# Optimization experiments

Hardware: AMD Instinct MI355X
Metric: run time of the kernel (lower is better)

The kernel has to match this reference:

```python
import jax, jax.numpy as jnp
import numpy as np

B, S, D, H = 2, 2048, 1024, 16
EPS = 1e-7  # keras backend epsilon

def setup_inputs() -> dict:
    key = jax.random.key(0)
    ks = jax.random.split(key, 5)
    x = jax.random.normal(ks[0], (B, S, D), dtype=jnp.float32)
    # mem_mask convention: attend where mem_mask == 0 (causal here)
    i = jnp.arange(S)
    causal = (i[None, :] > i[:, None]).astype(jnp.float32)  # 1 = masked
    mem_mask = jnp.broadcast_to(causal[None, None], (B, 1, S, S))
    Wqkv = jax.random.normal(ks[1], (D, 3 * D), dtype=jnp.float32) * (D ** -0.5)
    W_out = jax.random.normal(ks[2], (D, D), dtype=jnp.float32) * (D ** -0.5)
    b_out = jnp.zeros((D,), dtype=jnp.float32)
    scale = jnp.ones((D,), dtype=jnp.float32)
    gate = jax.random.normal(ks[3], (D,), dtype=jnp.float32) * 0.02
    return {"x": x, "mem_mask": mem_mask, "Wqkv": Wqkv, "W_out": W_out,
            "b_out": b_out, "scale": scale, "gate": gate}

def reference(x, mem_mask, Wqkv, W_out, b_out, scale, gate):
    b, s, d = x.shape
    dh = d // H
    h = jnp.einsum('bsd,de->bse', x, Wqkv)
    q, k, v = jnp.split(h, 3, axis=-1)
    def split_heads(t):
        return t.reshape(b, s, H, dh).transpose(0, 2, 1, 3)  # [B,H,S,dh]
    q, k, v = split_heads(q), split_heads(k), split_heads(v)
    q = q * (dh ** -0.5)
    logits = jnp.einsum('bhqd,bhkd->bhqk', q, k)
    logits = logits * (mem_mask == 0.0).astype(logits.dtype)
    weights = jax.nn.relu(logits)
    o = jnp.einsum('bhqk,bhkd->bhqd', weights, v)
    o = o.transpose(0, 2, 1, 3).reshape(b, s, d)  # combine heads
    # Gated RMSNorm
    ms = jnp.mean(o * o, axis=-1, keepdims=True)
    o = scale * o * jax.lax.rsqrt(ms + EPS) * jax.nn.sigmoid(gate * o)
    return jnp.einsum('bsd,de->bse', o, W_out) + b_out
```

## Files before the change

### kernel.cpp

```cpp
#include <hip/hip_runtime.h>
#include <hip/hip_bf16.h>

typedef unsigned short u16;
typedef __attribute__((ext_vector_type(8))) short bf16x8;
typedef __attribute__((ext_vector_type(4))) short short4v;
typedef __attribute__((ext_vector_type(4))) float floatx4;
typedef __attribute__((ext_vector_type(2))) unsigned uint2v;

__device__ __forceinline__ float bf2f(u16 u) {
    unsigned v = ((unsigned)u) << 16;
    return __builtin_bit_cast(float, v);
}
__device__ __forceinline__ u16 f2bf(float f) {
    unsigned u = __builtin_bit_cast(unsigned, f);
    u += 0x7fffu + ((u >> 16) & 1u);
    return (u16)(u >> 16);
}

#define GLDS16(g, l)                                                             \
    __builtin_amdgcn_global_load_lds(                                            \
        (const __attribute__((address_space(1))) void*)(g),                      \
        (__attribute__((address_space(3))) void*)(l), 16, 0, 0)

__global__ __launch_bounds__(256) void prep(const float* __restrict__ x, u16* __restrict__ xb,
                                            const float* __restrict__ Wqkv, u16* __restrict__ WqkvT,
                                            const float* __restrict__ Wout, u16* __restrict__ WoutT) {
    __shared__ u16 t[32][33];
    int blk = blockIdx.x;
    if (blk < 4096) {
        const int i = blk * 256 + threadIdx.x;
        const floatx4 v = ((const floatx4*)x)[i];
        short4v o;
#pragma unroll
        for (int j = 0; j < 4; ++j) o[j] = (short)f2bf(v[j]);
        ((short4v*)xb)[i] = o;
        return;
    }
    const float* in; u16* out; int R, C, bx, by;
    if (blk < 4096 + 3072) { blk -= 4096; in = Wqkv; out = WqkvT; R = 1024; C = 3072; bx = blk % 96; by = blk / 96; }
    else                   { blk -= 7168; in = Wout; out = WoutT; R = 1024; C = 1024; bx = blk & 31; by = blk >> 5; }
    const int c0 = bx * 32, r0 = by * 32;
    const int xx = threadIdx.x & 31, yy = threadIdx.x >> 5;
#pragma unroll
    for (int i = 0; i < 32; i += 8) t[yy + i][xx] = f2bf(in[(size_t)(r0 + yy + i) * C + c0 + xx]);
    __syncthreads();
#pragma unroll
    for (int i = 0; i < 32; i += 8) out[(size_t)(c0 + yy + i) * R + r0 + xx] = t[xx][yy + i];
}

template <int TM, bool BIAS, typename OUT, bool VT>
__global__ __launch_bounds__(256) void gemm_bt(const u16* __restrict__ A, const u16* __restrict__ Bt,
                                               OUT* __restrict__ C, const float* __restrict__ bias,
                                               u16* __restrict__ vtp, int M, int N, int K) {
    constexpr int MI = TM / 32;
    __shared__ u16 sA[TM * 32];
    __shared__ u16 sB[128 * 32];
    const int tid = threadIdx.x;
    const int lane = tid & 63, wave = tid >> 6;
    const int l15 = lane & 15, quad = lane >> 4;
    const int row0 = blockIdx.y * TM, col0 = blockIdx.x * 128;
    const int wm = (wave & 1) * (TM / 2), wn = (wave >> 1) * 64;
    const int c_ = (tid & 3) << 3;
    floatx4 acc[MI][4] = {};
    for (int k0 = 0; k0 < K; k0 += 32) {
#pragma unroll
        for (int it = 0; it < 2; ++it) {
            const int idx = it * 256 + tid;
            const int r = idx >> 2;
            GLDS16(Bt + (size_t)(col0 + r) * K + k0 + c_, sB + idx * 8);
        }
#pragma unroll
        for (int it = 0; it < TM / 64; ++it) {
            const int idx = it * 256 + tid;
            const int r = idx >> 2;
            GLDS16(A + (size_t)(row0 + r) * K + k0 + c_, sA + idx * 8);
        }
        __syncthreads();
        bf16x8 af[MI], bfr[4];
#pragma unroll
        for (int i = 0; i < MI; ++i) af[i] = *(const bf16x8*)(sA + (wm + i * 16 + l15) * 32 + quad * 8);
#pragma unroll
        for (int j = 0; j < 4; ++j) bfr[j] = *(const bf16x8*)(sB + (wn + j * 16 + l15) * 32 + quad * 8);
#pragma unroll
        for (int i = 0; i < MI; ++i)
#pragma unroll
            for (int j = 0; j < 4; ++j)
                acc[i][j] = __builtin_amdgcn_mfma_f32_16x16x32_bf16(af[i], bfr[j], acc[i][j], 0, 0, 0);
        __syncthreads();
    }
#pragma unroll
    for (int i = 0; i < MI; ++i) {
#pragma unroll
        for (int j = 0; j < 4; ++j) {
            const int col = col0 + wn + j * 16 + l15;
            const int row = row0 + wm + i * 16 + quad * 4;
            const float b = BIAS ? bias[col] : 0.f;
            short4v pk;
#pragma unroll
            for (int r = 0; r < 4; ++r) {
                const float v = acc[i][j][r] + b;
                if constexpr (sizeof(OUT) == 2)
                    C[(size_t)(row + r) * N + col] = (OUT)f2bf(v);
                else
                    C[(size_t)(row + r) * N + col] = (OUT)v;
                if constexpr (VT) pk[r] = (short)f2bf(v * 0.125f);
            }
            if constexpr (VT) {
                if (col0 >= 2048) {
                    const int bb = row >> 11, s = row & 2047;
                    const int hd = (col - 2048) >> 6, dh = col & 63;
                    *(short4v*)(vtp + ((size_t)(bb * 16 + hd) * 64 + dh) * 2048 + s) = pk;
                }
            }
        }
    }
}

__device__ __forceinline__ void pack_store(floatx4 s, u16* dst, bool diag, int kgb, int qg) {
    float v0 = fmaxf(s[0], 0.f), v1 = fmaxf(s[1], 0.f);
    float v2 = fmaxf(s[2], 0.f), v3 = fmaxf(s[3], 0.f);
    if (diag) {
        if (kgb + 0 > qg) v0 = 0.f;
        if (kgb + 1 > qg) v1 = 0.f;
        if (kgb + 2 > qg) v2 = 0.f;
        if (kgb + 3 > qg) v3 = 0.f;
    }
    uint2v p;
    p.x = ((__builtin_bit_cast(unsigned, v0) + 0x8000u) >> 16) |
          ((__builtin_bit_cast(unsigned, v1) + 0x8000u) & 0xffff0000u);
    p.y = ((__builtin_bit_cast(unsigned, v2) + 0x8000u) >> 16) |
          ((__builtin_bit_cast(unsigned, v3) + 0x8000u) & 0xffff0000u);
    *(uint2v*)dst = p;
}

__global__ __launch_bounds__(256) void relu_attn(const u16* __restrict__ h, const u16* __restrict__ vt,
                                                 float* __restrict__ o) {
    __shared__ u16 sK[3][64 * 64];
    __shared__ u16 sV[3][64 * 64];
    __shared__ u16 sP[128 * 72];
    const int bid = blockIdx.x;
    const int pr = bid >> 5;
    const int bh = bid & 31;
    const int b = bh >> 4, hd = bh & 15;
    const int qtl = pr, qth = 31 - pr;
    const int tid = threadIdx.x, lane = tid & 63, wave = tid >> 6;
    const int l15 = lane & 15, quad = lane >> 4;
    const int swz = l15 & 7;

    bf16x8 qfl[2], qfh[2];
    {
        const u16* ql = h + (size_t)(b * 2048 + qtl * 64 + wave * 16 + l15) * 3072 + hd * 64;
        const u16* qh = h + (size_t)(b * 2048 + qth * 64 + wave * 16 + l15) * 3072 + hd * 64;
#pragma unroll
        for (int ks = 0; ks < 2; ++ks) {
            qfl[ks] = *(const bf16x8*)(ql + ks * 32 + quad * 8);
            qfh[ks] = *(const bf16x8*)(qh + ks * 32 + quad * 8);
        }
    }

    floatx4 accl[4] = {}, acch[4] = {};
    const u16* kbase = h + (size_t)(b * 2048) * 3072 + 1024 + hd * 64;
    const u16* vbase = vt + (size_t)bh * 64 * 2048;
    const int qg = wave * 16 + l15;

    const u16* kq[2]; const u16* vq[2]; int lo[2];
#pragma unroll
    for (int it = 0; it < 2; ++it) {
        const int idx = it * 256 + tid;
        const int r = idx >> 3;
        const int cg = (idx & 7) ^ (r & 7);
        kq[it] = kbase + (size_t)r * 3072 + cg * 8;
        vq[it] = vbase + (size_t)r * 2048 + cg * 8;
        lo[it] = idx * 8;
    }
    auto stage = [&](int bufi) {
#pragma unroll
        for (int it = 0; it < 2; ++it) {
            GLDS16(kq[it], &sK[bufi][lo[it]]);
            GLDS16(vq[it], &sV[bufi][lo[it]]);
            kq[it] += 64 * 3072;
            vq[it] += 64;
        }
    };

    stage(0);
    stage(1);
    int bc = 0, bn = 1, bs = 2;

    for (int kc = 0; kc <= qth; ++kc) {
        if (kc < qth) asm volatile("s_waitcnt vmcnt(4)" ::: "memory");
        else          asm volatile("s_waitcnt vmcnt(0)" ::: "memory");
        __builtin_amdgcn_s_barrier();
        asm volatile("" ::: "memory");
        __builtin_amdgcn_sched_barrier(0);
        if (kc + 2 <= qth) stage(bs);

        const u16* sKb = sK[bc];
        const u16* sVb = sV[bc];
        const bool lact = (kc <= qtl);
        const floatx4 z = {0.f, 0.f, 0.f, 0.f};
        __builtin_amdgcn_s_setprio(1);
#pragma unroll
        for (int mt = 0; mt < 4; ++mt) {
            const int R = mt * 16 + l15;
            const int cq = quad ^ swz;
            const bf16x8 kf0 = *(const bf16x8*)(sKb + R * 64 + cq * 8);
            const bf16x8 kf1 = *(const bf16x8*)(sKb + R * 64 + (cq ^ 4) * 8);
            const int kgb = mt * 16 + quad * 4;
            floatx4 s = __builtin_amdgcn_mfma_f32_16x16x32_bf16(kf0, qfh[0], z, 0, 0, 0);
            s = __builtin_amdgcn_mfma_f32_16x16x32_bf16(kf1, qfh[1], s, 0, 0, 0);
            pack_store(s, sP + (size_t)(64 + qg) * 72 + kgb, kc == qth, kgb, qg);
            if (lact) {
                floatx4 t = __builtin_amdgcn_mfma_f32_16x16x32_bf16(kf0, qfl[0], z, 0, 0, 0);
                t = __builtin_amdgcn_mfma_f32_16x16x32_bf16(kf1, qfl[1], t, 0, 0, 0);
                pack_store(t, sP + (size_t)qg * 72 + kgb, kc == qtl, kgb, qg);
            }
        }
#pragma unroll
        for (int kb = 0; kb < 2; ++kb) {
            const bf16x8 pfh = *(const bf16x8*)(sP + (size_t)(64 + wave * 16 + l15) * 72 + kb * 32 + quad * 8);
#pragma unroll
            for (int nt = 0; nt < 4; ++nt) {
                const int cv = ((kb << 2) | quad) ^ swz;
                const bf16x8 vf = *(const bf16x8*)(sVb + (nt * 16 + l15) * 64 + cv * 8);
                acch[nt] = __builtin_amdgcn_mfma_f32_16x16x32_bf16(pfh, vf, acch[nt], 0, 0, 0);
                if (lact) {
                    const bf16x8 pfl = *(const bf16x8*)(sP + (size_t)(wave * 16 + l15) * 72 + kb * 32 + quad * 8);
                    accl[nt] = __builtin_amdgcn_mfma_f32_16x16x32_bf16(pfl, vf, accl[nt], 0, 0, 0);
                }
            }
        }
        __builtin_amdgcn_s_setprio(0);
        int t_ = bc; bc = bn; bn = bs; bs = t_;
    }
#pragma unroll
    for (int nt = 0; nt < 4; ++nt) {
        const int col = hd * 64 + nt * 16 + l15;
        const int rl = qtl * 64 + wave * 16 + quad * 4;
        const int rh = qth * 64 + wave * 16 + quad * 4;
#pragma unroll
        for (int r = 0; r < 4; ++r) {
            o[(size_t)(b * 2048 + rl + r) * 1024 + col] = accl[nt][r];
            o[(size_t)(b * 2048 + rh + r) * 1024 + col] = acch[nt][r];
        }
    }
}

__global__ __launch_bounds__(256) void rms_gate(const float* __restrict__ o, const float* __restrict__ scale,
                                                const float* __restrict__ gate, u16* __restrict__ out) {
    const int row = blockIdx.x;
    const int tid = threadIdx.x;
    const floatx4* op = (const floatx4*)(o + (size_t)row * 1024);
    floatx4 v = op[tid];
    float ss = v[0] * v[0] + v[1] * v[1] + v[2] * v[2] + v[3] * v[3];
#pragma unroll
    for (int m = 32; m >= 1; m >>= 1) ss += __shfl_xor(ss, m, 64);
    __shared__ float red[4];
    if ((tid & 63) == 0) red[tid >> 6] = ss;
    __syncthreads();
    const float ms = (red[0] + red[1] + red[2] + red[3]) * (1.0f / 1024.0f);
    const float inv = rsqrtf(ms + 1e-7f);
    const int c = tid * 4;
#pragma unroll
    for (int j = 0; j < 4; ++j) {
        const float s = scale[c + j];
        const float g = gate[c + j];
        const float x = v[j];
        const float sig = 1.0f / (1.0f + __expf(-g * x));
        out[(size_t)row * 1024 + c + j] = f2bf(s * x * inv * sig);
    }
}

extern "C" void kernel_launch(void* const* d_in, const int* in_sizes, int n_in,
                              void* d_out, int out_size, void* d_ws, size_t ws_size,
                              hipStream_t stream) {
    const float* x     = (const float*)d_in[0];
    const float* Wqkv  = (const float*)d_in[2];
    const float* Wout  = (const float*)d_in[3];
    const float* bout  = (const float*)d_in[4];
    const float* scale = (const float*)d_in[5];
    const float* gate  = (const float*)d_in[6];
    float* out = (float*)d_out;

    char* p = (char*)d_ws;
    u16* xb    = (u16*)p; p += (size_t)4096 * 1024 * 2;
    u16* h     = (u16*)p; p += (size_t)4096 * 3072 * 2;
    u16* vt    = (u16*)p; p += (size_t)32 * 64 * 2048 * 2;
    u16* WqkvT = (u16*)p; p += (size_t)3072 * 1024 * 2;
    u16* WoutT = (u16*)p; p += (size_t)1024 * 1024 * 2;
    float* oat = (float*)p; p += (size_t)4096 * 1024 * 4;
    u16* onorm = (u16*)p; p += (size_t)4096 * 1024 * 2;

    prep<<<8192, 256, 0, stream>>>(x, xb, Wqkv, WqkvT, Wout, WoutT);
    gemm_bt<128, false, u16, true><<<dim3(24, 32), 256, 0, stream>>>(xb, WqkvT, h, nullptr, vt, 4096, 3072, 1024);
    relu_attn<<<512, 256, 0, stream>>>(h, vt, oat);
    rms_gate<<<4096, 256, 0, stream>>>(oat, scale, gate, onorm);
    gemm_bt<64, true, float, false><<<dim3(8, 64), 256, 0, stream>>>(onorm, WoutT, out, bout, nullptr, 4096, 1024, 1024);
}
```

Baseline: 219.7 us.

## Keep attention P fragments in registers via permlane swaps; retile output GEMM

The ReLU attention kernel no longer writes the ReLU'd score tile to shared memory and reads it back as the A operand for the PV matmul. It repacks the MFMA output fragments in registers with permlane32/permlane16 swaps, falling back to shuffles when those builtins are unavailable. This removes the sP LDS buffer and its store/load traffic. The output projection GEMM is also retiled from 64x128 to 128x64 blocks via a new BN template parameter, which changes the grid shape and per-wave work. The register repack adds cross-lane ops and register pressure, and it relies on the fragment layout mapping being correct.

After: 216.2 us. Within noise of the previous version (-1.6%).

```diff
diff --git a/kernel.cpp b/kernel.cpp
--- a/kernel.cpp
+++ b/kernel.cpp
@@ -6,6 +6,7 @@
 typedef __attribute__((ext_vector_type(4))) short short4v;
 typedef __attribute__((ext_vector_type(4))) float floatx4;
 typedef __attribute__((ext_vector_type(2))) unsigned uint2v;
+typedef __attribute__((ext_vector_type(4))) unsigned uint4v;
 
 __device__ __forceinline__ float bf2f(u16 u) {
     unsigned v = ((unsigned)u) << 16;
@@ -21,6 +22,29 @@
     __builtin_amdgcn_global_load_lds(                                            \
         (const __attribute__((address_space(1))) void*)(g),                      \
         (__attribute__((address_space(3))) void*)(l), 16, 0, 0)
+
+__device__ __forceinline__ uint2v pl32(unsigned a, unsigned b) {
+#if __has_builtin(__builtin_amdgcn_permlane32_swap)
+    auto r = __builtin_amdgcn_permlane32_swap(a, b, false, false);
+    uint2v o; o.x = (unsigned)r[0]; o.y = (unsigned)r[1]; return o;
+#else
+    unsigned as = (unsigned)__shfl_xor((int)a, 32, 64);
+    unsigned bs = (unsigned)__shfl_xor((int)b, 32, 64);
+    const bool hi = (threadIdx.x & 32) != 0;
+    uint2v o; o.x = hi ? bs : a; o.y = hi ? b : as; return o;
+#endif
+}
+__device__ __forceinline__ uint2v pl16(unsigned a, unsigned b) {
+#if __has_builtin(__builtin_amdgcn_permlane16_swap)
+    auto r = __builtin_amdgcn_permlane16_swap(a, b, false, false);
+    uint2v o; o.x = (unsigned)r[0]; o.y = (unsigned)r[1]; return o;
+#else
+    unsigned as = (unsigned)__shfl_xor((int)a, 16, 64);
+    unsigned bs = (unsigned)__shfl_xor((int)b, 16, 64);
+    const bool odd = (threadIdx.x & 16) != 0;
+    uint2v o; o.x = odd ? bs : a; o.y = odd ? b : as; return o;
+#endif
+}
 
 __global__ __launch_bounds__(256) void prep(const float* __restrict__ x, u16* __restrict__ xb,
                                             const float* __restrict__ Wqkv, u16* __restrict__ WqkvT,
@@ -48,23 +72,24 @@
     for (int i = 0; i < 32; i += 8) out[(size_t)(c0 + yy + i) * R + r0 + xx] = t[xx][yy + i];
 }
 
-template <int TM, bool BIAS, typename OUT, bool VT>
+template <int TM, int BN, bool BIAS, typename OUT, bool VT>
 __global__ __launch_bounds__(256) void gemm_bt(const u16* __restrict__ A, const u16* __restrict__ Bt,
                                                OUT* __restrict__ C, const float* __restrict__ bias,
                                                u16* __restrict__ vtp, int M, int N, int K) {
     constexpr int MI = TM / 32;
+    constexpr int NJ = BN / 32;
     __shared__ u16 sA[TM * 32];
-    __shared__ u16 sB[128 * 32];
+    __shared__ u16 sB[BN * 32];
     const int tid = threadIdx.x;
     const int lane = tid & 63, wave = tid >> 6;
     const int l15 = lane & 15, quad = lane >> 4;
-    const int row0 = blockIdx.y * TM, col0 = blockIdx.x * 128;
-    const int wm = (wave & 1) * (TM / 2), wn = (wave >> 1) * 64;
+    const int row0 = blockIdx.y * TM, col0 = blockIdx.x * BN;
+    const int wm = (wave & 1) * (TM / 2), wn = (wave >> 1) * (BN / 2);
     const int c_ = (tid & 3) << 3;
-    floatx4 acc[MI][4] = {};
+    floatx4 acc[MI][NJ] = {};
     for (int k0 = 0; k0 < K; k0 += 32) {
 #pragma unroll
-        for (int it = 0; it < 2; ++it) {
+        for (int it = 0; it < BN / 64; ++it) {
             const int idx = it * 256 + tid;
             const int r = idx >> 2;
             GLDS16(Bt + (size_t)(col0 + r) * K + k0 + c_, sB + idx * 8);
@@ -76,22 +101,22 @@
             GLDS16(A + (size_t)(row0 + r) * K + k0 + c_, sA + idx * 8);
         }
         __syncthreads();
-        bf16x8 af[MI], bfr[4];
+        bf16x8 af[MI], bfr[NJ];
 #pragma unroll
         for (int i = 0; i < MI; ++i) af[i] = *(const bf16x8*)(sA + (wm + i * 16 + l15) * 32 + quad * 8);
 #pragma unroll
-        for (int j = 0; j < 4; ++j) bfr[j] = *(const bf16x8*)(sB + (wn + j * 16 + l15) * 32 + quad * 8);
+        for (int j = 0; j < NJ; ++j) bfr[j] = *(const bf16x8*)(sB + (wn + j * 16 + l15) * 32 + quad * 8);
 #pragma unroll
         for (int i = 0; i < MI; ++i)
 #pragma unroll
-            for (int j = 0; j < 4; ++j)
+            for (int j = 0; j < NJ; ++j)
                 acc[i][j] = __builtin_amdgcn_mfma_f32_16x16x32_bf16(af[i], bfr[j], acc[i][j], 0, 0, 0);
         __syncthreads();
     }
 #pragma unroll
     for (int i = 0; i < MI; ++i) {
 #pragma unroll
-        for (int j = 0; j < 4; ++j) {
+        for (int j = 0; j < NJ; ++j) {
             const int col = col0 + wn + j * 16 + l15;
             const int row = row0 + wm + i * 16 + quad * 4;
             const float b = BIAS ? bias[col] : 0.f;
@@ -116,7 +141,7 @@
     }
 }
 
-__device__ __forceinline__ void pack_store(floatx4 s, u16* dst, bool diag, int kgb, int qg) {
+__device__ __forceinline__ uint2v pack_relu(floatx4 s, bool diag, int kgb, int qg) {
     float v0 = fmaxf(s[0], 0.f), v1 = fmaxf(s[1], 0.f);
     float v2 = fmaxf(s[2], 0.f), v3 = fmaxf(s[3], 0.f);
     if (diag) {
@@ -130,14 +155,22 @@
           ((__builtin_bit_cast(unsigned, v1) + 0x8000u) & 0xffff0000u);
     p.y = ((__builtin_bit_cast(unsigned, v2) + 0x8000u) >> 16) |
           ((__builtin_bit_cast(unsigned, v3) + 0x8000u) & 0xffff0000u);
-    *(uint2v*)dst = p;
+    return p;
+}
+
+__device__ __forceinline__ bf16x8 pfrag(uint2v A, uint2v B) {
+    uint2v gx = pl32(A.x, B.x);
+    uint2v dx = pl16(gx.x, gx.y);
+    uint2v gy = pl32(A.y, B.y);
+    uint2v dy = pl16(gy.x, gy.y);
+    uint4v w; w.x = dx.x; w.y = dy.x; w.z = dx.y; w.w = dy.y;
+    return __builtin_bit_cast(bf16x8, w);
 }
 
 __global__ __launch_bounds__(256) void relu_attn(const u16* __restrict__ h, const u16* __restrict__ vt,
                                                  float* __restrict__ o) {
     __shared__ u16 sK[3][64 * 64];
     __shared__ u16 sV[3][64 * 64];
-    __shared__ u16 sP[128 * 72];
     const int bid = blockIdx.x;
     const int pr = bid >> 5;
     const int bh = bid & 31;
@@ -200,6 +233,7 @@
         const bool lact = (kc <= qtl);
         const floatx4 z = {0.f, 0.f, 0.f, 0.f};
         __builtin_amdgcn_s_setprio(1);
+        uint2v ph[4], pl_[4];
 #pragma unroll
         for (int mt = 0; mt < 4; ++mt) {
             const int R = mt * 16 + l15;
@@ -209,25 +243,24 @@
             const int kgb = mt * 16 + quad * 4;
             floatx4 s = __builtin_amdgcn_mfma_f32_16x16x32_bf16(kf0, qfh[0], z, 0, 0, 0);
             s = __builtin_amdgcn_mfma_f32_16x16x32_bf16(kf1, qfh[1], s, 0, 0, 0);
-            pack_store(s, sP + (size_t)(64 + qg) * 72 + kgb, kc == qth, kgb, qg);
+            ph[mt] = pack_relu(s, kc == qth, kgb, qg);
             if (lact) {
                 floatx4 t = __builtin_amdgcn_mfma_f32_16x16x32_bf16(kf0, qfl[0], z, 0, 0, 0);
                 t = __builtin_amdgcn_mfma_f32_16x16x32_bf16(kf1, qfl[1], t, 0, 0, 0);
-                pack_store(t, sP + (size_t)qg * 72 + kgb, kc == qtl, kgb, qg);
+                pl_[mt] = pack_relu(t, kc == qtl, kgb, qg);
             }
         }
 #pragma unroll
         for (int kb = 0; kb < 2; ++kb) {
-            const bf16x8 pfh = *(const bf16x8*)(sP + (size_t)(64 + wave * 16 + l15) * 72 + kb * 32 + quad * 8);
+            const bf16x8 pfh = pfrag(ph[2 * kb], ph[2 * kb + 1]);
+            bf16x8 pfl;
+            if (lact) pfl = pfrag(pl_[2 * kb], pl_[2 * kb + 1]);
 #pragma unroll
             for (int nt = 0; nt < 4; ++nt) {
                 const int cv = ((kb << 2) | quad) ^ swz;
                 const bf16x8 vf = *(const bf16x8*)(sVb + (nt * 16 + l15) * 64 + cv * 8);
                 acch[nt] = __builtin_amdgcn_mfma_f32_16x16x32_bf16(pfh, vf, acch[nt], 0, 0, 0);
-                if (lact) {
-                    const bf16x8 pfl = *(const bf16x8*)(sP + (size_t)(wave * 16 + l15) * 72 + kb * 32 + quad * 8);
-                    accl[nt] = __builtin_amdgcn_mfma_f32_16x16x32_bf16(pfl, vf, accl[nt], 0, 0, 0);
-                }
+                if (lact) accl[nt] = __builtin_amdgcn_mfma_f32_16x16x32_bf16(pfl, vf, accl[nt], 0, 0, 0);
             }
         }
         __builtin_amdgcn_s_setprio(0);
@@ -292,8 +325,8 @@
     u16* onorm = (u16*)p; p += (size_t)4096 * 1024 * 2;
 
     prep<<<8192, 256, 0, stream>>>(x, xb, Wqkv, WqkvT, Wout, WoutT);
-    gemm_bt<128, false, u16, true><<<dim3(24, 32), 256, 0, stream>>>(xb, WqkvT, h, nullptr, vt, 4096, 3072, 1024);
+    gemm_bt<128, 128, false, u16, true><<<dim3(24, 32), 256, 0, stream>>>(xb, WqkvT, h, nullptr, vt, 4096, 3072, 1024);
     relu_attn<<<512, 256, 0, stream>>>(h, vt, oat);
     rms_gate<<<4096, 256, 0, stream>>>(oat, scale, gate, onorm);
-    gemm_bt<64, true, float, false><<<dim3(8, 64), 256, 0, stream>>>(onorm, WoutT, out, bout, nullptr, 4096, 1024, 1024);
-}
+    gemm_bt<128, 64, true, float, false><<<dim3(16, 32), 256, 0, stream>>>(onorm, WoutT, out, bout, nullptr, 4096, 1024, 1024);
+}
```
